# Optimization experiments

Measured on AMD Instinct MI355X. Metric: run time of the kernel, lower is better.

The kernel has to match this reference:

```python
import jax, jax.numpy as jnp
import numpy as np

LOG_DUR_SCALE = 2.3  # durations ~ exp(U(0,2.3)) - 1, avg ~3 frames/phoneme


def setup_inputs() -> dict:
    key = jax.random.key(0)
    k1, k2 = jax.random.split(key)
    B, S, D = 32, 512, 384
    x = jax.random.normal(k1, (B, S, D), dtype=jnp.float32)
    log_duration_prediction = jax.random.uniform(k2, (B, S), dtype=jnp.float32) * LOG_DUR_SCALE
    return {"x": x, "log_duration_prediction": log_duration_prediction, "max_len": 3072}


def reference(x, log_duration_prediction, max_len):
    # duration_rounded = clamp(round(exp(logd) - 1), min=0)
    duration_rounded = jnp.clip(jnp.round(jnp.exp(log_duration_prediction) - 1.0), 0.0)
    dur = duration_rounded.astype(jnp.int32)                      # [B, S]
    cum = jnp.cumsum(dur, axis=1)                                 # [B, S] end offsets
    mel_len = jnp.minimum(cum[:, -1], max_len)                    # [B]
    t = jnp.arange(max_len, dtype=jnp.int32)                      # [T]
    # source index for output frame t: first phoneme whose cumulative end > t
    idx = jax.vmap(lambda c: jnp.searchsorted(c, t, side="right"))(cum)  # [B, T]
    idx = jnp.clip(idx, 0, x.shape[1] - 1)
    out = jnp.take_along_axis(x, idx[..., None], axis=1)          # [B, T, D]
    valid = t[None, :] < mel_len[:, None]                         # [B, T]
    out = jnp.where(valid[..., None], out, jnp.zeros((), out.dtype))
    mel_mask = ~valid  # get_mask_from_lengths: True at padding positions
    return out, duration_rounded, mel_len.astype(jnp.int32), mel_mask
```

## Files before the change

### kernel.cpp

```cpp
#include <hip/hip_runtime.h>

#define B 32
#define S 512
#define D 384
#define T 3072
#define FPB 32
#define D4 (D/4)

#define OFF_OUT  0
#define OFF_DUR  (B*T*D)
#define OFF_MLEN (OFF_DUR + B*S)
#define OFF_MASK (OFF_MLEN + B)

__global__ __launch_bounds__(512) void durations_kernel(
    const float* __restrict__ logd, const int* __restrict__ max_len_p,
    float* __restrict__ out, int* __restrict__ cum_ws, int* __restrict__ mlen_ws)
{
    const int b = blockIdx.x;
    const int s = threadIdx.x;

    float ld = logd[b * S + s];
    float dr = rintf(expf(ld) - 1.0f);
    dr = fmaxf(dr, 0.0f);
    int d = (int)dr;

    out[OFF_DUR + b * S + s] = dr;

    const int lane = s & 63;
    const int wave = s >> 6;
    int v = d;
    #pragma unroll
    for (int off = 1; off < 64; off <<= 1) {
        int u = __shfl_up(v, off, 64);
        if (lane >= off) v += u;
    }
    __shared__ int wsum[8];
    if (lane == 63) wsum[wave] = v;
    __syncthreads();
    if (s == 0) {
        int acc = 0;
        #pragma unroll
        for (int w = 0; w < 8; ++w) { int t = wsum[w]; wsum[w] = acc; acc += t; }
    }
    __syncthreads();
    const int cum = v + wsum[wave];
    cum_ws[b * S + s] = cum;

    if (s == S - 1) {
        int ml = min(cum, max_len_p[0]);
        mlen_ws[b] = ml;
        out[OFF_MLEN + b] = (float)ml;
    }
}

__global__ __launch_bounds__(256) void gather_kernel(
    const float* __restrict__ x, const int* __restrict__ cum_ws,
    const int* __restrict__ mlen_ws, float* __restrict__ outp)
{
    __shared__ int cum_s[S];
    __shared__ int sidx[FPB];
    __shared__ int mlen_s;

    const int b   = blockIdx.y;
    const int t0  = blockIdx.x * FPB;
    const int tid = threadIdx.x;

    for (int i = tid; i < S; i += 256) cum_s[i] = cum_ws[b * S + i];
    if (tid == 0) mlen_s = mlen_ws[b];
    __syncthreads();
    const int mlen = mlen_s;

    if (tid < FPB) {
        const int t = t0 + tid;
        int lo = 0;
        if (t < mlen) {
            int hi = S;
            while (lo < hi) {
                int mid = (lo + hi) >> 1;
                if (cum_s[mid] <= t) lo = mid + 1; else hi = mid;
            }
            if (lo > S - 1) lo = S - 1;
        }
        sidx[tid] = lo;
        outp[OFF_MASK + (size_t)b * T + t] = (t < mlen) ? 0.0f : 1.0f;
    }
    __syncthreads();

    const float4* x4 = (const float4*)(x + (size_t)b * S * D);
    float4* o4 = (float4*)(outp + OFF_OUT + (size_t)b * T * D + (size_t)t0 * D);

    #pragma unroll
    for (int i = 0; i < (FPB * D4) / 256; ++i) {
        int w = tid + i * 256;
        int f = w / D4;
        int e = w - f * D4;
        int t = t0 + f;
        float4 val;
        if (t < mlen) {
            val = x4[(size_t)sidx[f] * D4 + e];
        } else {
            val = make_float4(0.f, 0.f, 0.f, 0.f);
        }
        o4[(size_t)f * D4 + e] = val;
    }
}

extern "C" void kernel_launch(void* const* d_in, const int* in_sizes, int n_in,
                              void* d_out, int out_size, void* d_ws, size_t ws_size,
                              hipStream_t stream) {
    const float* x      = (const float*)d_in[0];
    const float* logd   = (const float*)d_in[1];
    const int*   maxlen = (const int*)d_in[2];
    float* out = (float*)d_out;

    int* cum_ws  = (int*)d_ws;
    int* mlen_ws = cum_ws + B * S;

    durations_kernel<<<B, 512, 0, stream>>>(logd, maxlen, out, cum_ws, mlen_ws);
    gather_kernel<<<dim3(T / FPB, B), 256, 0, stream>>>(x, cum_ws, mlen_ws, out);
}
```

Baseline: 34.97 us.

## Fuse duration scan into gather kernel and use nontemporal stores

Removes the separate durations kernel. Every gather block now recomputes the exp/round durations and the prefix scan for its batch row directly in shared memory, so the workspace round trip and one kernel launch go away. Output and mask writes switch to nontemporal stores to avoid cache pollution on the large streaming write. The cost is redundant scan work in all 96 blocks per batch row. Only blockIdx.x==0 writes the duration and mel_len outputs.

```diff
diff --git a/kernel.cpp b/kernel.cpp
--- a/kernel.cpp
+++ b/kernel.cpp
@@ -6,69 +6,64 @@
 #define T 3072
 #define FPB 32
 #define D4 (D/4)
+#define NTHREADS 256
+
+typedef float f32x4 __attribute__((ext_vector_type(4)));
 
 #define OFF_OUT  0
 #define OFF_DUR  (B*T*D)
 #define OFF_MLEN (OFF_DUR + B*S)
 #define OFF_MASK (OFF_MLEN + B)
 
-__global__ __launch_bounds__(512) void durations_kernel(
-    const float* __restrict__ logd, const int* __restrict__ max_len_p,
-    float* __restrict__ out, int* __restrict__ cum_ws, int* __restrict__ mlen_ws)
+__global__ __launch_bounds__(NTHREADS) void upsample_kernel(
+    const float* __restrict__ x, const float* __restrict__ logd,
+    const int* __restrict__ max_len_p, float* __restrict__ outp)
 {
-    const int b = blockIdx.x;
-    const int s = threadIdx.x;
+    __shared__ int cum_s[S];
+    __shared__ int wsum[NTHREADS / 64];
+    __shared__ int sidx[FPB];
+    __shared__ int mlen_sh;
 
-    float ld = logd[b * S + s];
-    float dr = rintf(expf(ld) - 1.0f);
-    dr = fmaxf(dr, 0.0f);
-    int d = (int)dr;
+    const int b   = blockIdx.y;
+    const int t0  = blockIdx.x * FPB;
+    const int tid = threadIdx.x;
+    const int lane = tid & 63;
+    const int wave = tid >> 6;
 
-    out[OFF_DUR + b * S + s] = dr;
+    const int s0 = tid * 2;
+    const float* ldrow = logd + b * S;
+    float ld0 = ldrow[s0], ld1 = ldrow[s0 + 1];
+    float dr0 = fmaxf(rintf(expf(ld0) - 1.0f), 0.0f);
+    float dr1 = fmaxf(rintf(expf(ld1) - 1.0f), 0.0f);
+    int d1 = (int)dr1;
+    int pairsum = (int)dr0 + d1;
 
-    const int lane = s & 63;
-    const int wave = s >> 6;
-    int v = d;
+    int v = pairsum;
     #pragma unroll
     for (int off = 1; off < 64; off <<= 1) {
         int u = __shfl_up(v, off, 64);
         if (lane >= off) v += u;
     }
-    __shared__ int wsum[8];
     if (lane == 63) wsum[wave] = v;
     __syncthreads();
-    if (s == 0) {
+    if (tid == 0) {
         int acc = 0;
         #pragma unroll
-        for (int w = 0; w < 8; ++w) { int t = wsum[w]; wsum[w] = acc; acc += t; }
+        for (int w = 0; w < NTHREADS / 64; ++w) { int t = wsum[w]; wsum[w] = acc; acc += t; }
     }
     __syncthreads();
-    const int cum = v + wsum[wave];
-    cum_ws[b * S + s] = cum;
+    const int inc  = v + wsum[wave];
+    cum_s[s0]     = inc - d1;
+    cum_s[s0 + 1] = inc;
 
-    if (s == S - 1) {
-        int ml = min(cum, max_len_p[0]);
-        mlen_ws[b] = ml;
-        out[OFF_MLEN + b] = (float)ml;
+    if (blockIdx.x == 0) {
+        outp[OFF_DUR + b * S + s0]     = dr0;
+        outp[OFF_DUR + b * S + s0 + 1] = dr1;
     }
-}
-
-__global__ __launch_bounds__(256) void gather_kernel(
-    const float* __restrict__ x, const int* __restrict__ cum_ws,
-    const int* __restrict__ mlen_ws, float* __restrict__ outp)
-{
-    __shared__ int cum_s[S];
-    __shared__ int sidx[FPB];
-    __shared__ int mlen_s;
-
-    const int b   = blockIdx.y;
-    const int t0  = blockIdx.x * FPB;
-    const int tid = threadIdx.x;
-
-    for (int i = tid; i < S; i += 256) cum_s[i] = cum_ws[b * S + i];
-    if (tid == 0) mlen_s = mlen_ws[b];
+    if (tid == NTHREADS - 1) mlen_sh = min(inc, max_len_p[0]);
     __syncthreads();
-    const int mlen = mlen_s;
+    const int mlen = mlen_sh;
+    if (blockIdx.x == 0 && tid == 0) outp[OFF_MLEN + b] = (float)mlen;
 
     if (tid < FPB) {
         const int t = t0 + tid;
@@ -82,26 +77,23 @@
             if (lo > S - 1) lo = S - 1;
         }
         sidx[tid] = lo;
-        outp[OFF_MASK + (size_t)b * T + t] = (t < mlen) ? 0.0f : 1.0f;
+        __builtin_nontemporal_store((t < mlen) ? 0.0f : 1.0f,
+                                    &outp[OFF_MASK + (size_t)b * T + t]);
     }
     __syncthreads();
 
-    const float4* x4 = (const float4*)(x + (size_t)b * S * D);
-    float4* o4 = (float4*)(outp + OFF_OUT + (size_t)b * T * D + (size_t)t0 * D);
+    const f32x4* x4 = (const f32x4*)(x + (size_t)b * S * D);
+    f32x4* o4 = (f32x4*)(outp + OFF_OUT + (size_t)b * T * D + (size_t)t0 * D);
 
     #pragma unroll
-    for (int i = 0; i < (FPB * D4) / 256; ++i) {
-        int w = tid + i * 256;
+    for (int i = 0; i < (FPB * D4) / NTHREADS; ++i) {
+        int w = tid + i * NTHREADS;
         int f = w / D4;
         int e = w - f * D4;
         int t = t0 + f;
-        float4 val;
-        if (t < mlen) {
-            val = x4[(size_t)sidx[f] * D4 + e];
-        } else {
-            val = make_float4(0.f, 0.f, 0.f, 0.f);
-        }
-        o4[(size_t)f * D4 + e] = val;
+        f32x4 val = (f32x4)(0.f);
+        if (t < mlen) val = x4[(size_t)sidx[f] * D4 + e];
+        __builtin_nontemporal_store(val, &o4[(size_t)f * D4 + e]);
     }
 }
 
@@ -113,9 +105,5 @@
     const int*   maxlen = (const int*)d_in[2];
     float* out = (float*)d_out;
 
-    int* cum_ws  = (int*)d_ws;
-    int* mlen_ws = cum_ws + B * S;
-
-    durations_kernel<<<B, 512, 0, stream>>>(logd, maxlen, out, cum_ws, mlen_ws);
-    gather_kernel<<<dim3(T / FPB, B), 256, 0, stream>>>(x, cum_ws, mlen_ws, out);
+    upsample_kernel<<<dim3(T / FPB, B), NTHREADS, 0, stream>>>(x, logd, maxlen, out);
 }
```

After: 36.41 us. +4.1%, slower.

## Scatter frame indices in duration kernel, swizzle gather blocks, use nontemporal stores

Applied to the files above, without the earlier changes.

The first kernel now writes the source phoneme index for every output frame directly, so the gather kernel no longer loads the cumulative array into shared memory or runs a per-frame binary search. The gather kernel processes 64 frames per block, remaps block IDs across 8 XCDs, and writes output with nontemporal stores to cut cache pollution on the large streaming write. The index scatter runs serially per thread over each phoneme's duration, and the workspace grows to B*T ints.

```diff
diff --git a/kernel.cpp b/kernel.cpp
--- a/kernel.cpp
+++ b/kernel.cpp
@@ -4,26 +4,31 @@
 #define S 512
 #define D 384
 #define T 3072
-#define FPB 32
+#define FPB 64
 #define D4 (D/4)
+#define NT 256
+#define BPR (T/FPB)
+#define NBLK (BPR*B)
+#define NXCD 8
+
+typedef float f32x4 __attribute__((ext_vector_type(4)));
 
 #define OFF_OUT  0
 #define OFF_DUR  (B*T*D)
 #define OFF_MLEN (OFF_DUR + B*S)
 #define OFF_MASK (OFF_MLEN + B)
 
+
 __global__ __launch_bounds__(512) void durations_kernel(
     const float* __restrict__ logd, const int* __restrict__ max_len_p,
-    float* __restrict__ out, int* __restrict__ cum_ws, int* __restrict__ mlen_ws)
+    float* __restrict__ out, int* __restrict__ idx_ws, int* __restrict__ mlen_ws)
 {
     const int b = blockIdx.x;
     const int s = threadIdx.x;
 
     float ld = logd[b * S + s];
-    float dr = rintf(expf(ld) - 1.0f);
-    dr = fmaxf(dr, 0.0f);
+    float dr = fmaxf(rintf(expf(ld) - 1.0f), 0.0f);
     int d = (int)dr;
-
     out[OFF_DUR + b * S + s] = dr;
 
     const int lane = s & 63;
@@ -43,65 +48,54 @@
         for (int w = 0; w < 8; ++w) { int t = wsum[w]; wsum[w] = acc; acc += t; }
     }
     __syncthreads();
-    const int cum = v + wsum[wave];
-    cum_ws[b * S + s] = cum;
+    const int inc = v + wsum[wave];
+    const int start = inc - d;
+    const int end = min(inc, T);
+    for (int t = start; t < end; ++t) idx_ws[b * T + t] = s;
 
     if (s == S - 1) {
-        int ml = min(cum, max_len_p[0]);
+        int ml = min(inc, max_len_p[0]);
         mlen_ws[b] = ml;
         out[OFF_MLEN + b] = (float)ml;
     }
 }
 
-__global__ __launch_bounds__(256) void gather_kernel(
-    const float* __restrict__ x, const int* __restrict__ cum_ws,
+__global__ __launch_bounds__(NT) void gather_kernel(
+    const float* __restrict__ x, const int* __restrict__ idx_ws,
     const int* __restrict__ mlen_ws, float* __restrict__ outp)
 {
-    __shared__ int cum_s[S];
     __shared__ int sidx[FPB];
-    __shared__ int mlen_s;
+    __shared__ int mlen_sh;
 
-    const int b   = blockIdx.y;
-    const int t0  = blockIdx.x * FPB;
+    const int lin = blockIdx.x;
+    const int swz = (lin & (NXCD - 1)) * (NBLK / NXCD) + (lin >> 3);
+    const int b   = swz / BPR;
+    const int t0  = (swz % BPR) * FPB;
     const int tid = threadIdx.x;
 
-    for (int i = tid; i < S; i += 256) cum_s[i] = cum_ws[b * S + i];
-    if (tid == 0) mlen_s = mlen_ws[b];
+    if (tid == 0) mlen_sh = mlen_ws[b];
+    if (tid < FPB) sidx[tid] = idx_ws[b * T + t0 + tid];
     __syncthreads();
-    const int mlen = mlen_s;
+    const int mlen = mlen_sh;
 
     if (tid < FPB) {
         const int t = t0 + tid;
-        int lo = 0;
-        if (t < mlen) {
-            int hi = S;
-            while (lo < hi) {
-                int mid = (lo + hi) >> 1;
-                if (cum_s[mid] <= t) lo = mid + 1; else hi = mid;
-            }
-            if (lo > S - 1) lo = S - 1;
-        }
-        sidx[tid] = lo;
-        outp[OFF_MASK + (size_t)b * T + t] = (t < mlen) ? 0.0f : 1.0f;
+        __builtin_nontemporal_store((t < mlen) ? 0.0f : 1.0f,
+                                    &outp[OFF_MASK + (size_t)b * T + t]);
     }
-    __syncthreads();
 
-    const float4* x4 = (const float4*)(x + (size_t)b * S * D);
-    float4* o4 = (float4*)(outp + OFF_OUT + (size_t)b * T * D + (size_t)t0 * D);
+    const f32x4* x4 = (const f32x4*)(x + (size_t)b * S * D);
+    f32x4* o4 = (f32x4*)(outp + OFF_OUT + (size_t)b * T * D + (size_t)t0 * D);
 
     #pragma unroll
-    for (int i = 0; i < (FPB * D4) / 256; ++i) {
-        int w = tid + i * 256;
+    for (int i = 0; i < (FPB * D4) / NT; ++i) {
+        int w = tid + i * NT;
         int f = w / D4;
         int e = w - f * D4;
         int t = t0 + f;
-        float4 val;
-        if (t < mlen) {
-            val = x4[(size_t)sidx[f] * D4 + e];
-        } else {
-            val = make_float4(0.f, 0.f, 0.f, 0.f);
-        }
-        o4[(size_t)f * D4 + e] = val;
+        f32x4 val = (f32x4)(0.f);
+        if (t < mlen) val = x4[(size_t)sidx[f] * D4 + e];
+        __builtin_nontemporal_store(val, &o4[(size_t)f * D4 + e]);
     }
 }
 
@@ -113,9 +107,9 @@
     const int*   maxlen = (const int*)d_in[2];
     float* out = (float*)d_out;
 
-    int* cum_ws  = (int*)d_ws;
-    int* mlen_ws = cum_ws + B * S;
+    int* idx_ws  = (int*)d_ws;
+    int* mlen_ws = idx_ws + B * T;
 
-    durations_kernel<<<B, 512, 0, stream>>>(logd, maxlen, out, cum_ws, mlen_ws);
-    gather_kernel<<<dim3(T / FPB, B), 256, 0, stream>>>(x, cum_ws, mlen_ws, out);
+    durations_kernel<<<B, 512, 0, stream>>>(logd, maxlen, out, idx_ws, mlen_ws);
+    gather_kernel<<<NBLK, NT, 0, stream>>>(x, idx_ws, mlen_ws, out);
 }
```

Result: slower. 39.18 us (+12.0%).
